# Performance work log

Measured on AMD Instinct MI355X. Metric: run time of the kernel, lower is better.

Reference implementation:

```python
import jax, jax.numpy as jnp
import numpy as np

N, K, C_IN, C_OUT = 100000, 16, 64, 64


def setup_inputs() -> dict:
    key = jax.random.key(0)
    ks = jax.random.split(key, 9)
    coords = jax.random.normal(ks[0], (N, 3), dtype=jnp.float32)
    features = jax.random.normal(ks[1], (N, C_IN), dtype=jnp.float32)
    idx = jax.random.randint(ks[2], (N, K), 0, N, dtype=jnp.int64)
    # kernel_mlp: Linear(3+C_IN, C_OUT) -> GELU -> Linear(C_OUT, C_OUT)
    s1 = 1.0 / np.sqrt(3 + C_IN)
    s2 = 1.0 / np.sqrt(C_OUT)
    W1 = jax.random.uniform(ks[3], (3 + C_IN, C_OUT), jnp.float32, -s1, s1)
    b1 = jax.random.uniform(ks[4], (C_OUT,), jnp.float32, -s1, s1)
    W2 = jax.random.uniform(ks[5], (C_OUT, C_OUT), jnp.float32, -s2, s2)
    b2 = jax.random.uniform(ks[6], (C_OUT,), jnp.float32, -s2, s2)
    sc = 1.0 / np.sqrt(C_IN)
    Ws = jax.random.uniform(ks[7], (C_IN, C_OUT), jnp.float32, -sc, sc)
    bs = jax.random.uniform(ks[8], (C_OUT,), jnp.float32, -sc, sc)
    return {"coords": coords, "features": features, "idx": idx,
            "W1": W1, "b1": b1, "W2": W2, "b2": b2, "Ws": Ws, "bs": bs}


def reference(coords, features, idx, W1, b1, W2, b2, Ws, bs):
    # gather neighbors: [N, K, 3] and [N, K, C_IN]
    neighbor_coords = coords[idx]
    neighbor_features = features[idx]
    rel_pos = neighbor_coords - coords[:, None, :]
    kernel_input = jnp.concatenate([rel_pos, neighbor_features], axis=-1)  # [N, K, 3+C_IN]
    h = jax.nn.gelu(kernel_input @ W1 + b1, approximate=False)  # torch GELU is exact erf
    kernel_out = h @ W2 + b2  # [N, K, C_OUT]
    aggregated = kernel_out.mean(axis=1)  # [N, C_OUT]
    return aggregated + features @ Ws + bs
```

## Files before the change

kernel.cpp:

```cpp
#include <hip/hip_runtime.h>
#include <hip/hip_fp16.h>
#include <math.h>


#define KNN 16

typedef _Float16 half8 __attribute__((ext_vector_type(8)));
typedef float float4v __attribute__((ext_vector_type(4)));

__device__ __forceinline__ float lane_bcast(float v, int lane) {
    return __int_as_float(__builtin_amdgcn_readlane(__float_as_int(v), lane));
}

__device__ __forceinline__ float gelu_fast(float x) {
    const float t = x * fmaf(x * x, -0.10294324f, -2.30220821f);
    return x * __builtin_amdgcn_rcpf(1.0f + exp2f(t));
}

__global__ __launch_bounds__(256) void gno_phase1(
    const float* __restrict__ features, const float* __restrict__ coords,
    const float* __restrict__ W1, const float* __restrict__ b1,
    const float* __restrict__ Ws, const float* __restrict__ bs,
    const float* __restrict__ b2, __half* __restrict__ Gp,
    float* __restrict__ out, int n)
{
    const int c = threadIdx.x;
    float w1r[64], wsr[64];
    #pragma unroll
    for (int d = 0; d < 64; ++d) {
        w1r[d] = W1[(3 + d) * 64 + c];
        wsr[d] = Ws[d * 64 + c];
    }
    const float w1px = W1[c], w1py = W1[64 + c], w1pz = W1[128 + c];
    const float b1c = b1[c];
    const float sbc = bs[c] + b2[c];

    const int wave   = blockIdx.x * 4 + threadIdx.y;
    const int stride = gridDim.x * 4;
    for (int i0 = wave * 2; i0 < n; i0 += stride * 2) {
        const int i1 = i0 + 1;
        const bool has1 = (i1 < n);
        const float f0 = features[(size_t)i0 * 64 + c];
        const float f1 = has1 ? features[(size_t)i1 * 64 + c] : 0.0f;

        float a0 = fmaf(coords[(size_t)i0 * 3 + 0], w1px, b1c);
        a0 = fmaf(coords[(size_t)i0 * 3 + 1], w1py, a0);
        a0 = fmaf(coords[(size_t)i0 * 3 + 2], w1pz, a0);
        float a1 = b1c;
        if (has1) {
            a1 = fmaf(coords[(size_t)i1 * 3 + 0], w1px, a1);
            a1 = fmaf(coords[(size_t)i1 * 3 + 1], w1py, a1);
            a1 = fmaf(coords[(size_t)i1 * 3 + 2], w1pz, a1);
        }
        float s0 = sbc, s1 = sbc;
        #pragma unroll
        for (int d = 0; d < 64; ++d) {
            const float fd0 = lane_bcast(f0, d);
            const float fd1 = lane_bcast(f1, d);
            a0 = fmaf(fd0, w1r[d], a0);
            s0 = fmaf(fd0, wsr[d], s0);
            a1 = fmaf(fd1, w1r[d], a1);
            s1 = fmaf(fd1, wsr[d], s1);
        }
        Gp[(size_t)i0 * 64 + c]  = __float2half(a0);
        out[(size_t)i0 * 64 + c] = s0;
        if (has1) {
            Gp[(size_t)i1 * 64 + c]  = __float2half(a1);
            out[(size_t)i1 * 64 + c] = s1;
        }
    }
}

__global__ __launch_bounds__(256, 4) void gno_phase2(
    const float* __restrict__ coords, const int* __restrict__ idx,
    const float* __restrict__ W1, const float* __restrict__ W2,
    const __half2* __restrict__ Gp2, float* __restrict__ out, int n)
{
    __shared__ unsigned short w2h[4096];
    __shared__ unsigned short hbarall[4][1024];

    const int tid = threadIdx.y * 64 + threadIdx.x;
    for (int t = tid; t < 4096; t += 256)
        w2h[t] = __half_as_ushort(__float2half(W2[t]));

    const int c   = threadIdx.x;
    const int m   = c & 31;
    const int odd = c >> 5;
    const int p16 = c & 15;
    const int l4  = c >> 4;
    const float wx0 = W1[2 * m],       wx1 = W1[2 * m + 1];
    const float wy0 = W1[64 + 2 * m],  wy1 = W1[64 + 2 * m + 1];
    const float wz0 = W1[128 + 2 * m], wz1 = W1[128 + 2 * m + 1];
    __syncthreads();

    half8 bf[4][2];
    #pragma unroll
    for (int t = 0; t < 4; ++t)
        #pragma unroll
        for (int h = 0; h < 2; ++h)
            #pragma unroll
            for (int j = 0; j < 8; ++j)
                bf[t][h][j] = *(const _Float16*)&w2h[(h * 32 + l4 * 8 + j) * 64 + t * 16 + p16];

    unsigned short* hb = hbarall[threadIdx.y];

    const int ngroups = n >> 4;
    const int gw = blockIdx.x * 4 + threadIdx.y;
    const int nw = gridDim.x * 4;
    for (int g = gw; g < ngroups; g += nw) {
        const int gbase = g << 4;
        #pragma unroll 2
        for (int pp = 0; pp < 8; ++pp) {
            const int i0 = gbase + 2 * pp;
            const int i1 = i0 + 1;
            const int vj = idx[i0 * KNN + (c & 31)];

            const float c0x = coords[(size_t)i0 * 3 + 0];
            const float c0y = coords[(size_t)i0 * 3 + 1];
            const float c0z = coords[(size_t)i0 * 3 + 2];
            const float c1x = coords[(size_t)i1 * 3 + 0];
            const float c1y = coords[(size_t)i1 * 3 + 1];
            const float c1z = coords[(size_t)i1 * 3 + 2];
            float P00 = c0x * wx0; P00 = fmaf(c0y, wy0, P00); P00 = fmaf(c0z, wz0, P00);
            float P01 = c0x * wx1; P01 = fmaf(c0y, wy1, P01); P01 = fmaf(c0z, wz1, P01);
            float P10 = c1x * wx0; P10 = fmaf(c1y, wy0, P10); P10 = fmaf(c1z, wz0, P10);
            float P11 = c1x * wx1; P11 = fmaf(c1y, wy1, P11); P11 = fmaf(c1z, wz1, P11);

            __half2 gv[16];
            #pragma unroll
            for (int q = 0; q < 8; ++q) {
                const int se = __builtin_amdgcn_readlane(vj, 2 * q);
                const int so = __builtin_amdgcn_readlane(vj, 2 * q + 1);
                const int row = odd ? so : se;
                gv[q] = Gp2[(size_t)row * 32 + m];
            }
            #pragma unroll
            for (int q = 0; q < 8; ++q) {
                const int se = __builtin_amdgcn_readlane(vj, 16 + 2 * q);
                const int so = __builtin_amdgcn_readlane(vj, 17 + 2 * q);
                const int row = odd ? so : se;
                gv[8 + q] = Gp2[(size_t)row * 32 + m];
            }

            float a00 = 0.f, a01 = 0.f, a10 = 0.f, a11 = 0.f;
            #pragma unroll
            for (int q = 0; q < 8; ++q) {
                const float2 xy = __half22float2(gv[q]);
                a00 += gelu_fast(xy.x - P00);
                a01 += gelu_fast(xy.y - P01);
            }
            #pragma unroll
            for (int q = 0; q < 8; ++q) {
                const float2 xy = __half22float2(gv[8 + q]);
                a10 += gelu_fast(xy.x - P10);
                a11 += gelu_fast(xy.y - P11);
            }
            a00 *= (1.0f / KNN); a01 *= (1.0f / KNN);
            a10 *= (1.0f / KNN); a11 *= (1.0f / KNN);
            a00 += __shfl_xor(a00, 32, 64);
            a01 += __shfl_xor(a01, 32, 64);
            a10 += __shfl_xor(a10, 32, 64);
            a11 += __shfl_xor(a11, 32, 64);

            const int lp = 2 * pp + odd;
            const float x0 = odd ? a10 : a00;
            const float x1 = odd ? a11 : a01;
            __half2 hh = __floats2half2_rn(x0, x1);
            int byte = lp * 128 + m * 4;
            byte ^= (lp & 7) << 4;
            *(unsigned int*)((char*)hb + byte) = *(unsigned int*)&hh;
        }

        int b0 = p16 * 128 + l4 * 16;       b0 ^= (p16 & 7) << 4;
        int b1 = p16 * 128 + 64 + l4 * 16;  b1 ^= (p16 & 7) << 4;
        const half8 af0 = *(const half8*)((const char*)hb + b0);
        const half8 af1 = *(const half8*)((const char*)hb + b1);

        #pragma unroll
        for (int t = 0; t < 4; ++t) {
            float4v cf;
            #pragma unroll
            for (int j = 0; j < 4; ++j)
                cf[j] = out[(size_t)(gbase + l4 * 4 + j) * 64 + t * 16 + p16];
            float4v d = __builtin_amdgcn_mfma_f32_16x16x32_f16(af0, bf[t][0], cf, 0, 0, 0);
            d = __builtin_amdgcn_mfma_f32_16x16x32_f16(af1, bf[t][1], d, 0, 0, 0);
            #pragma unroll
            for (int j = 0; j < 4; ++j)
                out[(size_t)(gbase + l4 * 4 + j) * 64 + t * 16 + p16] = d[j];
        }
    }
}

extern "C" void kernel_launch(void* const* d_in, const int* in_sizes, int n_in,
                              void* d_out, int out_size, void* d_ws, size_t ws_size,
                              hipStream_t stream) {
    const float* coords   = (const float*)d_in[0];
    const float* features = (const float*)d_in[1];
    const int*   idx      = (const int*)d_in[2];
    const float* W1       = (const float*)d_in[3];
    const float* b1       = (const float*)d_in[4];
    const float* W2       = (const float*)d_in[5];
    const float* b2       = (const float*)d_in[6];
    const float* Ws       = (const float*)d_in[7];
    const float* bs       = (const float*)d_in[8];
    float* out = (float*)d_out;
    const int n = in_sizes[0] / 3;
    __half* Gp = (__half*)d_ws;

    dim3 block(64, 4);
    gno_phase1<<<dim3(1024), block, 0, stream>>>(features, coords, W1, b1,
                                                 Ws, bs, b2, Gp, out, n);
    gno_phase2<<<dim3(782),  block, 0, stream>>>(coords, idx, W1, W2,
                                                 (const __half2*)Gp, out, n);
}
```

Before: 209.9 us.

## Batch neighbor gathers four pairs deep and vectorize idx/coords loads per group

Phase 2 now loads all 256 neighbor indices for a 16-point group with a single int4 vector load per lane, and all 48 coords with one load per lane, then broadcasts them via readlane. It also issues 64 half2 gathers (four point pairs) before doing any GELU math, which deepens memory-level parallelism for the random gathers. In exchange it uses more registers, and the occupancy hint in launch bounds is lowered from 4 to 3 blocks per SIMD to allow that.

After: 201.7 us. -3.9%, faster.

```diff
diff --git a/kernel.cpp b/kernel.cpp
--- a/kernel.cpp
+++ b/kernel.cpp
@@ -7,6 +7,7 @@
 
 typedef _Float16 half8 __attribute__((ext_vector_type(8)));
 typedef float float4v __attribute__((ext_vector_type(4)));
+typedef int int4v __attribute__((ext_vector_type(4)));
 
 __device__ __forceinline__ float lane_bcast(float v, int lane) {
     return __int_as_float(__builtin_amdgcn_readlane(__float_as_int(v), lane));
@@ -71,7 +72,7 @@
     }
 }
 
-__global__ __launch_bounds__(256, 4) void gno_phase2(
+__global__ __launch_bounds__(256, 3) void gno_phase2(
     const float* __restrict__ coords, const int* __restrict__ idx,
     const float* __restrict__ W1, const float* __restrict__ W2,
     const __half2* __restrict__ Gp2, float* __restrict__ out, int n)
@@ -88,6 +89,7 @@
     const int odd = c >> 5;
     const int p16 = c & 15;
     const int l4  = c >> 4;
+    const int m4  = m * 4;
     const float wx0 = W1[2 * m],       wx1 = W1[2 * m + 1];
     const float wy0 = W1[64 + 2 * m],  wy1 = W1[64 + 2 * m + 1];
     const float wz0 = W1[128 + 2 * m], wz1 = W1[128 + 2 * m + 1];
@@ -103,72 +105,80 @@
                 bf[t][h][j] = *(const _Float16*)&w2h[(h * 32 + l4 * 8 + j) * 64 + t * 16 + p16];
 
     unsigned short* hb = hbarall[threadIdx.y];
+    const char* gpb = (const char*)Gp2;
 
     const int ngroups = n >> 4;
     const int gw = blockIdx.x * 4 + threadIdx.y;
     const int nw = gridDim.x * 4;
     for (int g = gw; g < ngroups; g += nw) {
         const int gbase = g << 4;
-        #pragma unroll 2
-        for (int pp = 0; pp < 8; ++pp) {
-            const int i0 = gbase + 2 * pp;
-            const int i1 = i0 + 1;
-            const int vj = idx[i0 * KNN + (c & 31)];
-
-            const float c0x = coords[(size_t)i0 * 3 + 0];
-            const float c0y = coords[(size_t)i0 * 3 + 1];
-            const float c0z = coords[(size_t)i0 * 3 + 2];
-            const float c1x = coords[(size_t)i1 * 3 + 0];
-            const float c1y = coords[(size_t)i1 * 3 + 1];
-            const float c1z = coords[(size_t)i1 * 3 + 2];
-            float P00 = c0x * wx0; P00 = fmaf(c0y, wy0, P00); P00 = fmaf(c0z, wz0, P00);
-            float P01 = c0x * wx1; P01 = fmaf(c0y, wy1, P01); P01 = fmaf(c0z, wz1, P01);
-            float P10 = c1x * wx0; P10 = fmaf(c1y, wy0, P10); P10 = fmaf(c1z, wz0, P10);
-            float P11 = c1x * wx1; P11 = fmaf(c1y, wy1, P11); P11 = fmaf(c1z, wz1, P11);
-
-            __half2 gv[16];
-            #pragma unroll
-            for (int q = 0; q < 8; ++q) {
-                const int se = __builtin_amdgcn_readlane(vj, 2 * q);
-                const int so = __builtin_amdgcn_readlane(vj, 2 * q + 1);
-                const int row = odd ? so : se;
-                gv[q] = Gp2[(size_t)row * 32 + m];
+        const int4v vj4 = *(const int4v*)(idx + (size_t)gbase * 16 + c * 4);
+        const float cv = (c < 48) ? coords[(size_t)gbase * 3 + c] : 0.0f;
+
+        #pragma unroll
+        for (int h = 0; h < 2; ++h) {
+            __half2 gv[4][16];
+            #pragma unroll
+            for (int pp = 0; pp < 4; ++pp) {
+                const int P2 = h * 4 + pp;
+                const int e0 = P2 * 32;
+                #pragma unroll
+                for (int q = 0; q < 8; ++q) {
+                    const int ea = e0 + 2 * q,      eb = ea + 1;
+                    const int ec = e0 + 16 + 2 * q, ed = ec + 1;
+                    const int se = __builtin_amdgcn_readlane(vj4[ea & 3], ea >> 2);
+                    const int so = __builtin_amdgcn_readlane(vj4[eb & 3], eb >> 2);
+                    const int te = __builtin_amdgcn_readlane(vj4[ec & 3], ec >> 2);
+                    const int td = __builtin_amdgcn_readlane(vj4[ed & 3], ed >> 2);
+                    const int rA = odd ? so : se;
+                    const int rB = odd ? td : te;
+                    gv[pp][q]     = *(const __half2*)(gpb + (((unsigned)rA << 7) + m4));
+                    gv[pp][8 + q] = *(const __half2*)(gpb + (((unsigned)rB << 7) + m4));
+                }
             }
             #pragma unroll
-            for (int q = 0; q < 8; ++q) {
-                const int se = __builtin_amdgcn_readlane(vj, 16 + 2 * q);
-                const int so = __builtin_amdgcn_readlane(vj, 17 + 2 * q);
-                const int row = odd ? so : se;
-                gv[8 + q] = Gp2[(size_t)row * 32 + m];
+            for (int pp = 0; pp < 4; ++pp) {
+                const int P2  = h * 4 + pp;
+                const int lp0 = 2 * P2;
+                const float a0x = lane_bcast(cv, 3 * lp0 + 0);
+                const float a0y = lane_bcast(cv, 3 * lp0 + 1);
+                const float a0z = lane_bcast(cv, 3 * lp0 + 2);
+                const float a1x = lane_bcast(cv, 3 * lp0 + 3);
+                const float a1y = lane_bcast(cv, 3 * lp0 + 4);
+                const float a1z = lane_bcast(cv, 3 * lp0 + 5);
+                float P00 = a0x * wx0; P00 = fmaf(a0y, wy0, P00); P00 = fmaf(a0z, wz0, P00);
+                float P01 = a0x * wx1; P01 = fmaf(a0y, wy1, P01); P01 = fmaf(a0z, wz1, P01);
+                float P10 = a1x * wx0; P10 = fmaf(a1y, wy0, P10); P10 = fmaf(a1z, wz0, P10);
+                float P11 = a1x * wx1; P11 = fmaf(a1y, wy1, P11); P11 = fmaf(a1z, wz1, P11);
+
+                float a00 = 0.f, a01 = 0.f, a10 = 0.f, a11 = 0.f;
+                #pragma unroll
+                for (int q = 0; q < 8; ++q) {
+                    const float2 xy = __half22float2(gv[pp][q]);
+                    a00 += gelu_fast(xy.x - P00);
+                    a01 += gelu_fast(xy.y - P01);
+                }
+                #pragma unroll
+                for (int q = 0; q < 8; ++q) {
+                    const float2 xy = __half22float2(gv[pp][8 + q]);
+                    a10 += gelu_fast(xy.x - P10);
+                    a11 += gelu_fast(xy.y - P11);
+                }
+                a00 *= (1.0f / KNN); a01 *= (1.0f / KNN);
+                a10 *= (1.0f / KNN); a11 *= (1.0f / KNN);
+                a00 += __shfl_xor(a00, 32, 64);
+                a01 += __shfl_xor(a01, 32, 64);
+                a10 += __shfl_xor(a10, 32, 64);
+                a11 += __shfl_xor(a11, 32, 64);
+
+                const int lp = lp0 + odd;
+                const float x0 = odd ? a10 : a00;
+                const float x1 = odd ? a11 : a01;
+                __half2 hh = __floats2half2_rn(x0, x1);
+                int byte = lp * 128 + m4;
+                byte ^= (lp & 7) << 4;
+                *(unsigned int*)((char*)hb + byte) = *(unsigned int*)&hh;
             }
-
-            float a00 = 0.f, a01 = 0.f, a10 = 0.f, a11 = 0.f;
-            #pragma unroll
-            for (int q = 0; q < 8; ++q) {
-                const float2 xy = __half22float2(gv[q]);
-                a00 += gelu_fast(xy.x - P00);
-                a01 += gelu_fast(xy.y - P01);
-            }
-            #pragma unroll
-            for (int q = 0; q < 8; ++q) {
-                const float2 xy = __half22float2(gv[8 + q]);
-                a10 += gelu_fast(xy.x - P10);
-                a11 += gelu_fast(xy.y - P11);
-            }
-            a00 *= (1.0f / KNN); a01 *= (1.0f / KNN);
-            a10 *= (1.0f / KNN); a11 *= (1.0f / KNN);
-            a00 += __shfl_xor(a00, 32, 64);
-            a01 += __shfl_xor(a01, 32, 64);
-            a10 += __shfl_xor(a10, 32, 64);
-            a11 += __shfl_xor(a11, 32, 64);
-
-            const int lp = 2 * pp + odd;
-            const float x0 = odd ? a10 : a00;
-            const float x1 = odd ? a11 : a01;
-            __half2 hh = __floats2half2_rn(x0, x1);
-            int byte = lp * 128 + m * 4;
-            byte ^= (lp & 7) << 4;
-            *(unsigned int*)((char*)hb + byte) = *(unsigned int*)&hh;
         }
 
         int b0 = p16 * 128 + l4 * 16;       b0 ^= (p16 & 7) << 4;
```
